# Optimization experiments

Hardware: AMD Instinct MI355X
Metric: run time of the kernel (lower is better)

The kernel has to match this reference:

```python
import jax, jax.numpy as jnp
import numpy as np

B, L, E, DK = 16, 2048, 1024, 128
MODE = "Decoder"


def setup_inputs() -> dict:
    key = jax.random.key(0)
    ks = jax.random.split(key, 6)
    x = jax.random.normal(ks[0], (B, L, E), dtype=jnp.float32)
    context = jax.random.normal(ks[1], (B, L, E), dtype=jnp.float32)
    batch_lengths = jax.random.randint(ks[2], (B,), 1, L + 1)  # valid lengths in [1, L]
    Wq = jax.random.normal(ks[3], (E, DK), dtype=jnp.float32) * 0.02
    Wk = jax.random.normal(ks[4], (E, DK), dtype=jnp.float32) * 0.02
    Wv = jax.random.normal(ks[5], (E, DK), dtype=jnp.float32) * 0.02
    return {"x": x, "context": context, "batch_lengths": batch_lengths,
            "Wq": Wq, "Wk": Wk, "Wv": Wv, "max_len": L}


def reference(x, context, batch_lengths, Wq, Wk, Wv, max_len):
    # x, context: [B, L, E]; batch_lengths: [B] ints; weights: [E, DK]
    Lq = x.shape[1]
    dk = Wq.shape[1]
    pos = jnp.arange(Lq)
    # outputMask: zero out padded time steps, broadcast over feature dim [B, L, 1]
    len_mask = (pos[None, :] < batch_lengths[:, None]).astype(x.dtype)[:, :, None]
    Q = (context @ Wq) * len_mask
    K = (context @ Wk) * len_mask
    V = (x @ Wv) * len_mask
    # energy: [B, Lq, Lk]
    energy = jnp.einsum("bqd,bkd->bqk", Q, K)
    # attnMask: -inf on padded key positions
    key_valid = pos[None, None, :] < batch_lengths[:, None, None]  # [B,1,Lk]
    if MODE == "Decoder":
        causal = pos[None, :, None] >= pos[None, None, :]  # j <= i
        key_valid = key_valid & causal
    energy = jnp.where(key_valid, energy, -jnp.inf)
    score = jax.nn.softmax(energy / jnp.sqrt(jnp.asarray(dk, x.dtype)), axis=-1)
    return jnp.einsum("bqk,bkd->bqd", score, V)
```

## Files before the change

kernel.cpp:

```cpp
#include <hip/hip_runtime.h>

#define DEV __device__ __forceinline__

typedef __attribute__((ext_vector_type(4))) float f32x4;
typedef __attribute__((ext_vector_type(4))) unsigned short u16x4;
typedef __attribute__((ext_vector_type(8))) __bf16 bf16x8;

constexpr int NB = 16, SL = 2048, EM = 1024, DKD = 128;

DEV unsigned short f2bf(float f) {
  unsigned int u = __float_as_uint(f);
  u += 0x7FFFu + ((u >> 16) & 1u);
  return (unsigned short)(u >> 16);
}

DEV f32x4 mfma16(bf16x8 a, bf16x8 b, f32x4 c) {
  return __builtin_amdgcn_mfma_f32_16x16x32_bf16(a, b, c, 0, 0, 0);
}

DEV void dma16(const void* g, void* l) {
  __builtin_amdgcn_global_load_lds(
      (const __attribute__((address_space(1))) unsigned int*)g,
      (__attribute__((address_space(3))) unsigned int*)l, 16, 0, 0);
}

DEV bf16x8 cvt8(f32x4 a, f32x4 b) {
  bf16x8 r;
  r[0] = (__bf16)a[0]; r[1] = (__bf16)a[1]; r[2] = (__bf16)a[2]; r[3] = (__bf16)a[3];
  r[4] = (__bf16)b[0]; r[5] = (__bf16)b[1]; r[6] = (__bf16)b[2]; r[7] = (__bf16)b[3];
  return r;
}

#define SBAR() __builtin_amdgcn_sched_barrier(0)

__global__ __launch_bounds__(256) void prep_w(
    const float* __restrict__ Wq, const float* __restrict__ Wk,
    const float* __restrict__ Wv, unsigned short* __restrict__ Wt,
    float* __restrict__ mvg)
{
  __shared__ unsigned short T[64 * 128];
  const int tid = threadIdx.x;
  if (blockIdx.x == 0) {
    #pragma unroll
    for (int i = 0; i < NB * DKD / 256; ++i) mvg[i * 256 + tid] = 0.f;
  }
  const int m = blockIdx.x >> 4, kc = blockIdx.x & 15;
  const float* W = (m == 0) ? Wq : ((m == 1) ? Wk : Wv);
  #pragma unroll
  for (int it = 0; it < 8; ++it) {
    int idx = it * 256 + tid;
    int kk = idx >> 5, n4 = (idx & 31) * 4;
    f32x4 w4 = *(const f32x4*)(W + (size_t)(kc * 64 + kk) * DKD + n4);
    *(u16x4*)&T[kk * 128 + n4] =
        u16x4{ f2bf(w4[0]), f2bf(w4[1]), f2bf(w4[2]), f2bf(w4[3]) };
  }
  __syncthreads();
  #pragma unroll
  for (int it = 0; it < 4; ++it) {
    int idx = it * 256 + tid;
    int p = idx & 7, n = idx >> 3;
    int c = p ^ (n & 7);
    unsigned short v[8];
    #pragma unroll
    for (int e = 0; e < 8; ++e) v[e] = T[(c * 8 + e) * 128 + n];
    size_t t = ((size_t)(m * 16 + kc) * 128 + n) * 8 + p;
    *(u16x4*)(Wt + t * 8)     = u16x4{v[0], v[1], v[2], v[3]};
    *(u16x4*)(Wt + t * 8 + 4) = u16x4{v[4], v[5], v[6], v[7]};
  }
}

__global__ __launch_bounds__(256, 2) void proj_qk(
    const float* __restrict__ ctx, const unsigned short* __restrict__ Wt,
    const int* __restrict__ lens, unsigned short* __restrict__ Qo,
    unsigned short* __restrict__ Kz)
{
  __shared__ float Als[2][64 * 64];
  const int tid = threadIdx.x;
  const int wave = tid >> 6, lane = tid & 63;
  const int quad = lane >> 4, mm = lane & 15;
  const int rb = blockIdx.x * 64;
  const int len = lens[blockIdx.x >> 5];
  if ((rb & (SL - 1)) >= len) return;

  f32x4 acc[4][4];
  #pragma unroll
  for (int i = 0; i < 4; ++i)
    #pragma unroll
    for (int j = 0; j < 4; ++j) acc[i][j] = f32x4{0.f, 0.f, 0.f, 0.f};

  const float* asrc[4];
  #pragma unroll
  for (int i = 0; i < 4; ++i) {
    const int rl_ = wave * 16 + i * 4 + (lane >> 4);
    const int cc  = (lane & 8) | ((lane & 7) ^ (rl_ & 7));
    asrc[i] = ctx + (size_t)(rb + rl_) * EM + cc * 4;
  }
  int soff[2][2];
  #pragma unroll
  for (int ks = 0; ks < 2; ++ks) {
    soff[ks][0] = (ks * 8 + ((quad * 2)     ^ (mm & 7))) * 4;
    soff[ks][1] = (ks * 8 + ((quad * 2 + 1) ^ (mm & 7))) * 4;
  }
  const unsigned short* bbase[4][2];
  #pragma unroll
  for (int lo = 0; lo < 4; ++lo)
    #pragma unroll
    for (int ks = 0; ks < 2; ++ks) {
      const int nrow = (wave * 4 + lo) * 16 + mm;
      const int pp = (ks * 4 + quad) ^ (mm & 7);
      const int cs = nrow * 8 + pp;
      bbase[lo][ks] = Wt + ((size_t)(cs >> 10) * 16384 + (cs & 1023)) * 8;
    }

  #pragma unroll
  for (int i = 0; i < 4; ++i)
    dma16(asrc[i],      (char*)Als[0] + wave * 4096 + i * 1024);
  #pragma unroll
  for (int i = 0; i < 4; ++i)
    dma16(asrc[i] + 64, (char*)Als[1] + wave * 4096 + i * 1024);
  __asm__ volatile("s_waitcnt vmcnt(4)" ::: "memory");
  __builtin_amdgcn_s_barrier();

  #pragma unroll 1
  for (int kc = 0; kc < 16; ++kc) {
    SBAR();
    bf16x8 bfr[4][2];
    #pragma unroll
    for (int lo = 0; lo < 4; ++lo)
      #pragma unroll
      for (int ks = 0; ks < 2; ++ks)
        bfr[lo][ks] = *(const bf16x8*)(bbase[lo][ks] + (size_t)kc * 8192);
    bf16x8 af[4][2];
    #pragma unroll
    for (int rt = 0; rt < 4; ++rt) {
      const float* rbase = Als[kc & 1] + (rt * 16 + mm) * 64;
      #pragma unroll
      for (int ks = 0; ks < 2; ++ks) {
        f32x4 a0 = *(const f32x4*)(rbase + soff[ks][0]);
        f32x4 a1 = *(const f32x4*)(rbase + soff[ks][1]);
        af[rt][ks] = cvt8(a0, a1);
      }
    }
    __asm__ volatile("s_waitcnt lgkmcnt(0)" ::: "memory");
    SBAR();
    __builtin_amdgcn_s_barrier();
    {
      const int kn = (kc + 2 < 16) ? (kc + 2) : 15;
      #pragma unroll
      for (int i = 0; i < 4; ++i)
        dma16(asrc[i] + kn * 64, (char*)Als[kc & 1] + wave * 4096 + i * 1024);
    }
    #pragma unroll
    for (int lo = 0; lo < 4; ++lo)
      #pragma unroll
      for (int ks = 0; ks < 2; ++ks)
        #pragma unroll
        for (int rt = 0; rt < 4; ++rt)
          acc[rt][lo] = mfma16(af[rt][ks], bfr[lo][ks], acc[rt][lo]);
    __builtin_amdgcn_s_barrier();
  }
  __asm__ volatile("s_waitcnt vmcnt(0)" ::: "memory");

  const float SCALE = 1.4426950408889634f * 0.08838834764831845f;
  #pragma unroll
  for (int rt = 0; rt < 4; ++rt)
    #pragma unroll
    for (int lo = 0; lo < 4; ++lo) {
      const int ctg = wave * 4 + lo;
      #pragma unroll
      for (int reg = 0; reg < 4; ++reg) {
        const int row = rb + rt * 16 + quad * 4 + reg;
        const int j = row & (SL - 1);
        const float val = acc[rt][lo][reg];
        if (ctg < 8) {
          const int d = ctg * 16 + mm;
          Qo[(size_t)row * DKD + d] = f2bf(val * ((j < len) ? SCALE : 0.f));
        } else {
          const int d = (ctg - 8) * 16 + mm;
          Kz[(size_t)row * DKD + (((d >> 3) ^ (j & 15)) * 8) + (d & 7)] = f2bf(val);
        }
      }
    }
}

__global__ __launch_bounds__(256, 2) void proj_v(
    const float* __restrict__ x, const unsigned short* __restrict__ Wt,
    const int* __restrict__ lens, unsigned short* __restrict__ Vz,
    float* __restrict__ mvg)
{
  __shared__ float Als[2][64 * 64];
  const int tid = threadIdx.x;
  const int wave = tid >> 6, lane = tid & 63;
  const int quad = lane >> 4, mm = lane & 15;
  const int rb = blockIdx.x * 64;
  const int bidx = blockIdx.x >> 5;
  const int len = lens[bidx];
  if ((rb & (SL - 1)) >= len) return;

  f32x4 acc[4][2];
  #pragma unroll
  for (int i = 0; i < 4; ++i) { acc[i][0] = f32x4{0.f,0.f,0.f,0.f}; acc[i][1] = f32x4{0.f,0.f,0.f,0.f}; }

  const float* asrc[4];
  #pragma unroll
  for (int i = 0; i < 4; ++i) {
    const int rl_ = wave * 16 + i * 4 + (lane >> 4);
    const int cc  = (lane & 8) | ((lane & 7) ^ (rl_ & 7));
    asrc[i] = x + (size_t)(rb + rl_) * EM + cc * 4;
  }
  int soff[2][2];
  #pragma unroll
  for (int ks = 0; ks < 2; ++ks) {
    soff[ks][0] = (ks * 8 + ((quad * 2)     ^ (mm & 7))) * 4;
    soff[ks][1] = (ks * 8 + ((quad * 2 + 1) ^ (mm & 7))) * 4;
  }
  const unsigned short* bbase[2][2];
  #pragma unroll
  for (int lo = 0; lo < 2; ++lo)
    #pragma unroll
    for (int ks = 0; ks < 2; ++ks) {
      const int nrow = (wave * 2 + lo) * 16 + mm;
      const int pp = (ks * 4 + quad) ^ (mm & 7);
      const int cs = nrow * 8 + pp;
      bbase[lo][ks] = Wt + ((size_t)2 * 16384 + cs) * 8;
    }

  #pragma unroll
  for (int i = 0; i < 4; ++i)
    dma16(asrc[i],      (char*)Als[0] + wave * 4096 + i * 1024);
  #pragma unroll
  for (int i = 0; i < 4; ++i)
    dma16(asrc[i] + 64, (char*)Als[1] + wave * 4096 + i * 1024);
  __asm__ volatile("s_waitcnt vmcnt(4)" ::: "memory");
  __builtin_amdgcn_s_barrier();

  #pragma unroll 1
  for (int kc = 0; kc < 16; ++kc) {
    SBAR();
    bf16x8 bfr[2][2];
    #pragma unroll
    for (int lo = 0; lo < 2; ++lo)
      #pragma unroll
      for (int ks = 0; ks < 2; ++ks)
        bfr[lo][ks] = *(const bf16x8*)(bbase[lo][ks] + (size_t)kc * 8192);
    bf16x8 af[4][2];
    #pragma unroll
    for (int rt = 0; rt < 4; ++rt) {
      const float* rbase = Als[kc & 1] + (rt * 16 + mm) * 64;
      #pragma unroll
      for (int ks = 0; ks < 2; ++ks) {
        f32x4 a0 = *(const f32x4*)(rbase + soff[ks][0]);
        f32x4 a1 = *(const f32x4*)(rbase + soff[ks][1]);
        af[rt][ks] = cvt8(a0, a1);
      }
    }
    __asm__ volatile("s_waitcnt lgkmcnt(0)" ::: "memory");
    SBAR();
    __builtin_amdgcn_s_barrier();
    {
      const int kn = (kc + 2 < 16) ? (kc + 2) : 15;
      #pragma unroll
      for (int i = 0; i < 4; ++i)
        dma16(asrc[i] + kn * 64, (char*)Als[kc & 1] + wave * 4096 + i * 1024);
    }
    #pragma unroll
    for (int lo = 0; lo < 2; ++lo)
      #pragma unroll
      for (int ks = 0; ks < 2; ++ks)
        #pragma unroll
        for (int rt = 0; rt < 4; ++rt)
          acc[rt][lo] = mfma16(af[rt][ks], bfr[lo][ks], acc[rt][lo]);
    __builtin_amdgcn_s_barrier();
  }
  __asm__ volatile("s_waitcnt vmcnt(0)" ::: "memory");

  #pragma unroll
  for (int rt = 0; rt < 4; ++rt)
    #pragma unroll
    for (int lo = 0; lo < 2; ++lo) {
      const int d = (wave * 2 + lo) * 16 + mm;
      const int row0 = rb + rt * 16 + quad * 4;
      const int b = row0 >> 11, j0 = row0 & (SL - 1);
      u16x4 pk = u16x4{ f2bf(acc[rt][lo][0]), f2bf(acc[rt][lo][1]),
                        f2bf(acc[rt][lo][2]), f2bf(acc[rt][lo][3]) };
      size_t off = (size_t)b * DKD * SL + (size_t)d * SL + (j0 & ~63)
                 + ((((j0 >> 3) & 7) ^ (d & 7)) * 8) + (j0 & 7);
      *(u16x4*)(Vz + off) = pk;
    }

  const int jb = rb & (SL - 1);
  #pragma unroll
  for (int lo = 0; lo < 2; ++lo) {
    const int d = (wave * 2 + lo) * 16 + mm;
    float part = 0.f;
    #pragma unroll
    for (int rt = 0; rt < 4; ++rt) {
      const int jr = jb + rt * 16 + quad * 4;
      #pragma unroll
      for (int reg = 0; reg < 4; ++reg)
        if (jr + reg < len) part += acc[rt][lo][reg];
    }
    part += __shfl_xor(part, 16);
    part += __shfl_xor(part, 32);
    if (quad == 0) atomicAdd(mvg + bidx * DKD + d, part);
  }
}

__global__ __launch_bounds__(256, 2) void attn(
    const unsigned short* __restrict__ Qw, const unsigned short* __restrict__ Kz,
    const unsigned short* __restrict__ Vz, const float* __restrict__ mvg,
    const int* __restrict__ lens, float* __restrict__ out)
{
  __shared__ unsigned short Ks[2][64 * 128];
  __shared__ unsigned short Vs[2][128 * 64];
  __shared__ unsigned short Ps[4][16 * 72];
  const int tid = threadIdx.x;
  const int wave = tid >> 6, lane = tid & 63;
  const int quad = lane >> 4, mm = lane & 15;
  const int b = blockIdx.y;
  const int qb = ((int)gridDim.x - 1 - (int)blockIdx.x) * 64;
  const int len = lens[b];

  if (qb >= len) {
    const int dd = (tid & 31) * 4;
    const int r0 = tid >> 5;
    const f32x4 m4 = *(const f32x4*)(mvg + b * DKD + dd);
    const float inv = 1.0f / (float)len;
    const f32x4 val = f32x4{ m4[0]*inv, m4[1]*inv, m4[2]*inv, m4[3]*inv };
    #pragma unroll
    for (int it = 0; it < 8; ++it) {
      const int row = qb + it * 8 + r0;
      *(f32x4*)(out + ((size_t)b * SL + row) * DKD + dd) = val;
    }
    return;
  }

  const int kend = min(qb + 64, len);
  const int nblk = (kend + 63) >> 6;
  const int irow0 = qb + wave * 16 + quad * 4;

  bf16x8 aQ[4];
  {
    const unsigned short* qbase =
        Qw + (size_t)(b * SL + qb + wave * 16 + mm) * DKD + quad * 8;
    #pragma unroll
    for (int cc = 0; cc < 4; ++cc) aQ[cc] = *(const bf16x8*)(qbase + cc * 32);
  }
  bf16x8 onesb;
  #pragma unroll
  for (int i = 0; i < 8; ++i) onesb[i] = (__bf16)1.0f;

  float mr[4];
  #pragma unroll
  for (int r = 0; r < 4; ++r) mr[r] = -__builtin_inff();
  f32x4 acc[8];
  #pragma unroll
  for (int i = 0; i < 8; ++i) acc[i] = f32x4{0.f,0.f,0.f,0.f};
  f32x4 accl = f32x4{0.f,0.f,0.f,0.f};

  #pragma unroll
  for (int it = 0; it < 4; ++it) {
    int s = it * 256 + tid;
    dma16(Kz + (size_t)(b * SL) * DKD + (size_t)s * 8,
          (char*)Ks[0] + (it * 256 + wave * 64) * 16);
  }
  #pragma unroll
  for (int it = 0; it < 4; ++it) {
    int s = it * 256 + tid;
    int d = s >> 3, p = s & 7;
    dma16(Vz + (size_t)b * DKD * SL + (size_t)d * SL + p * 8,
          (char*)Vs[0] + (it * 256 + wave * 64) * 16);
  }

  #pragma unroll 1
  for (int blk = 0; blk < nblk; ++blk) {
    const int kb = blk * 64;
    __syncthreads();
    if (blk + 1 < nblk) {
      const int kb1 = kb + 64;
      const int nb = (blk + 1) & 1;
      #pragma unroll
      for (int it = 0; it < 4; ++it) {
        int s = it * 256 + tid;
        dma16(Kz + (size_t)(b * SL + kb1) * DKD + (size_t)s * 8,
              (char*)Ks[nb] + (it * 256 + wave * 64) * 16);
      }
      #pragma unroll
      for (int it = 0; it < 4; ++it) {
        int s = it * 256 + tid;
        int d = s >> 3, p = s & 7;
        dma16(Vz + (size_t)b * DKD * SL + (size_t)d * SL + kb1 + p * 8,
              (char*)Vs[nb] + (it * 256 + wave * 64) * 16);
      }
    }
    const unsigned short* kbuf = Ks[blk & 1];
    const unsigned short* vbuf = Vs[blk & 1];

    f32x4 s4[4];
    #pragma unroll
    for (int nt = 0; nt < 4; ++nt) {
      f32x4 c = f32x4{0.f,0.f,0.f,0.f};
      const int j = nt * 16 + mm;
      #pragma unroll
      for (int cc = 0; cc < 4; ++cc) {
        const int pp = (cc * 4 + quad) ^ mm;
        bf16x8 kf = *(const bf16x8*)(kbuf + j * 128 + pp * 8);
        c = mfma16(aQ[cc], kf, c);
      }
      s4[nt] = c;
    }

    float alpha[4];
    #pragma unroll
    for (int reg = 0; reg < 4; ++reg) {
      const int jl = min(irow0 + reg + 1, len);
      float v0 = (kb + mm      < jl) ? s4[0][reg] : -__builtin_inff();
      float v1 = (kb + 16 + mm < jl) ? s4[1][reg] : -__builtin_inff();
      float v2 = (kb + 32 + mm < jl) ? s4[2][reg] : -__builtin_inff();
      float v3 = (kb + 48 + mm < jl) ? s4[3][reg] : -__builtin_inff();
      float mx = fmaxf(fmaxf(v0, v1), fmaxf(v2, v3));
      #pragma unroll
      for (int xm = 1; xm < 16; xm <<= 1) mx = fmaxf(mx, __shfl_xor(mx, xm));
      const float mn = fmaxf(mr[reg], mx);
      alpha[reg] = __builtin_amdgcn_exp2f(mr[reg] - mn);
      const float p0 = __builtin_amdgcn_exp2f(v0 - mn);
      const float p1 = __builtin_amdgcn_exp2f(v1 - mn);
      const float p2 = __builtin_amdgcn_exp2f(v2 - mn);
      const float p3 = __builtin_amdgcn_exp2f(v3 - mn);
      mr[reg] = mn;
      const int prow = quad * 4 + reg;
      Ps[wave][prow * 72 + mm]      = f2bf(p0);
      Ps[wave][prow * 72 + 16 + mm] = f2bf(p1);
      Ps[wave][prow * 72 + 32 + mm] = f2bf(p2);
      Ps[wave][prow * 72 + 48 + mm] = f2bf(p3);
    }
    #pragma unroll
    for (int nt = 0; nt < 8; ++nt) {
      f32x4 a = acc[nt];
      a[0] *= alpha[0]; a[1] *= alpha[1]; a[2] *= alpha[2]; a[3] *= alpha[3];
      acc[nt] = a;
    }
    accl[0] *= alpha[0]; accl[1] *= alpha[1];
    accl[2] *= alpha[2]; accl[3] *= alpha[3];
    __asm__ volatile("s_waitcnt lgkmcnt(0)" ::: "memory");
    bf16x8 aP[2];
    #pragma unroll
    for (int ks = 0; ks < 2; ++ks)
      aP[ks] = *(const bf16x8*)(&Ps[wave][mm * 72 + ks * 32 + quad * 8]);
    #pragma unroll
    for (int ks = 0; ks < 2; ++ks) {
      #pragma unroll
      for (int nt = 0; nt < 8; ++nt) {
        const int pp = (ks * 4 + quad) ^ (mm & 7);
        bf16x8 vf = *(const bf16x8*)(vbuf + (nt * 16 + mm) * 64 + pp * 8);
        acc[nt] = mfma16(aP[ks], vf, acc[nt]);
      }
      accl = mfma16(aP[ks], onesb, accl);
    }
  }

  #pragma unroll
  for (int reg = 0; reg < 4; ++reg) {
    const float rl = 1.0f / accl[reg];
    const size_t base = ((size_t)b * SL + irow0 + reg) * DKD + mm;
    #pragma unroll
    for (int nt = 0; nt < 8; ++nt)
      out[base + nt * 16] = acc[nt][reg] * rl;
  }
}

extern "C" void kernel_launch(void* const* d_in, const int* in_sizes, int n_in,
                              void* d_out, int out_size, void* d_ws, size_t ws_size,
                              hipStream_t stream) {
  const float* x    = (const float*)d_in[0];
  const float* ctx  = (const float*)d_in[1];
  const int*   lens = (const int*)d_in[2];
  const float* Wq   = (const float*)d_in[3];
  const float* Wk   = (const float*)d_in[4];
  const float* Wv   = (const float*)d_in[5];
  float* out = (float*)d_out;

  const size_t QKV = (size_t)NB * SL * DKD * sizeof(unsigned short);
  const size_t WTSZ = (size_t)3 * 16 * 128 * 8 * 8 * sizeof(unsigned short);
  const size_t MVSZ = (size_t)NB * DKD * sizeof(float);
  if (ws_size < 3 * QKV + WTSZ + MVSZ) return;
  unsigned short* Qws = (unsigned short*)d_ws;
  unsigned short* Kzs = (unsigned short*)((char*)d_ws + QKV);
  unsigned short* Vzs = (unsigned short*)((char*)d_ws + 2 * QKV);
  unsigned short* Wt  = (unsigned short*)((char*)d_ws + 3 * QKV);
  float*          mvg = (float*)((char*)d_ws + 3 * QKV + WTSZ);

  prep_w <<<dim3(48), 256, 0, stream>>>(Wq, Wk, Wv, Wt, mvg);
  proj_qk<<<dim3(NB * SL / 64), 256, 0, stream>>>(ctx, Wt, lens, Qws, Kzs);
  proj_v <<<dim3(NB * SL / 64), 256, 0, stream>>>(x, Wt, lens, Vzs, mvg);
  attn   <<<dim3(SL / 64, NB), 256, 0, stream>>>(Qws, Kzs, Vzs, mvg, lens, out);
}
```

Measured before the change: 346.8 us.

## Split attention keys across two wave groups and drop LDS staging in projections

The projection kernels stop staging activations in LDS through DMA and barriers. Each wave now loads fp32 rows from global memory into registers with one-step prefetch and uses a 2x2 wave tiling over rows and columns. The attention kernel goes to 512 threads: two wave groups each handle half of a 128-key block, and their partial softmax states are merged through LDS at the end. It also adds s_setprio around the MFMA sections and clamps the running max so fully masked halves do not produce NaN. The cost is more LDS for K/V and more register pressure, and projection reads lose LDS reuse and may be less coalesced.

```diff
diff --git a/kernel.cpp b/kernel.cpp
--- a/kernel.cpp
+++ b/kernel.cpp
@@ -30,8 +30,6 @@
   r[4] = (__bf16)b[0]; r[5] = (__bf16)b[1]; r[6] = (__bf16)b[2]; r[7] = (__bf16)b[3];
   return r;
 }
-
-#define SBAR() __builtin_amdgcn_sched_barrier(0)
 
 __global__ __launch_bounds__(256) void prep_w(
     const float* __restrict__ Wq, const float* __restrict__ Wk,
@@ -74,109 +72,83 @@
     const int* __restrict__ lens, unsigned short* __restrict__ Qo,
     unsigned short* __restrict__ Kz)
 {
-  __shared__ float Als[2][64 * 64];
   const int tid = threadIdx.x;
   const int wave = tid >> 6, lane = tid & 63;
   const int quad = lane >> 4, mm = lane & 15;
+  const int mh = wave >> 1, nh = wave & 1;
   const int rb = blockIdx.x * 64;
   const int len = lens[blockIdx.x >> 5];
   if ((rb & (SL - 1)) >= len) return;
 
-  f32x4 acc[4][4];
-  #pragma unroll
-  for (int i = 0; i < 4; ++i)
-    #pragma unroll
-    for (int j = 0; j < 4; ++j) acc[i][j] = f32x4{0.f, 0.f, 0.f, 0.f};
-
-  const float* asrc[4];
-  #pragma unroll
-  for (int i = 0; i < 4; ++i) {
-    const int rl_ = wave * 16 + i * 4 + (lane >> 4);
-    const int cc  = (lane & 8) | ((lane & 7) ^ (rl_ & 7));
-    asrc[i] = ctx + (size_t)(rb + rl_) * EM + cc * 4;
-  }
-  int soff[2][2];
-  #pragma unroll
-  for (int ks = 0; ks < 2; ++ks) {
-    soff[ks][0] = (ks * 8 + ((quad * 2)     ^ (mm & 7))) * 4;
-    soff[ks][1] = (ks * 8 + ((quad * 2 + 1) ^ (mm & 7))) * 4;
-  }
-  const unsigned short* bbase[4][2];
-  #pragma unroll
-  for (int lo = 0; lo < 4; ++lo)
+  f32x4 acc[2][8];
+  #pragma unroll
+  for (int rt = 0; rt < 2; ++rt)
+    #pragma unroll
+    for (int nt = 0; nt < 8; ++nt) acc[rt][nt] = f32x4{0.f, 0.f, 0.f, 0.f};
+
+  const float* arow[2];
+  #pragma unroll
+  for (int rt = 0; rt < 2; ++rt)
+    arow[rt] = ctx + (size_t)(rb + mh * 32 + rt * 16 + mm) * EM + quad * 8;
+
+  const int pl0 = (quad)     ^ (mm & 7);
+  const int pl1 = (4 + quad) ^ (mm & 7);
+  const unsigned short* bb = Wt + (size_t)nh * 131072 + mm * 64;
+
+  f32x4 An[2][2][2];
+  #pragma unroll
+  for (int rt = 0; rt < 2; ++rt)
     #pragma unroll
     for (int ks = 0; ks < 2; ++ks) {
-      const int nrow = (wave * 4 + lo) * 16 + mm;
-      const int pp = (ks * 4 + quad) ^ (mm & 7);
-      const int cs = nrow * 8 + pp;
-      bbase[lo][ks] = Wt + ((size_t)(cs >> 10) * 16384 + (cs & 1023)) * 8;
-    }
-
-  #pragma unroll
-  for (int i = 0; i < 4; ++i)
-    dma16(asrc[i],      (char*)Als[0] + wave * 4096 + i * 1024);
-  #pragma unroll
-  for (int i = 0; i < 4; ++i)
-    dma16(asrc[i] + 64, (char*)Als[1] + wave * 4096 + i * 1024);
-  __asm__ volatile("s_waitcnt vmcnt(4)" ::: "memory");
-  __builtin_amdgcn_s_barrier();
+      An[rt][ks][0] = *(const f32x4*)(arow[rt] + ks * 32);
+      An[rt][ks][1] = *(const f32x4*)(arow[rt] + ks * 32 + 4);
+    }
 
   #pragma unroll 1
   for (int kc = 0; kc < 16; ++kc) {
-    SBAR();
-    bf16x8 bfr[4][2];
-    #pragma unroll
-    for (int lo = 0; lo < 4; ++lo)
+    bf16x8 af[2][2];
+    #pragma unroll
+    for (int rt = 0; rt < 2; ++rt)
       #pragma unroll
       for (int ks = 0; ks < 2; ++ks)
-        bfr[lo][ks] = *(const bf16x8*)(bbase[lo][ks] + (size_t)kc * 8192);
-    bf16x8 af[4][2];
-    #pragma unroll
-    for (int rt = 0; rt < 4; ++rt) {
-      const float* rbase = Als[kc & 1] + (rt * 16 + mm) * 64;
-      #pragma unroll
-      for (int ks = 0; ks < 2; ++ks) {
-        f32x4 a0 = *(const f32x4*)(rbase + soff[ks][0]);
-        f32x4 a1 = *(const f32x4*)(rbase + soff[ks][1]);
-        af[rt][ks] = cvt8(a0, a1);
-      }
-    }
-    __asm__ volatile("s_waitcnt lgkmcnt(0)" ::: "memory");
-    SBAR();
-    __builtin_amdgcn_s_barrier();
-    {
-      const int kn = (kc + 2 < 16) ? (kc + 2) : 15;
-      #pragma unroll
-      for (int i = 0; i < 4; ++i)
-        dma16(asrc[i] + kn * 64, (char*)Als[kc & 1] + wave * 4096 + i * 1024);
-    }
-    #pragma unroll
-    for (int lo = 0; lo < 4; ++lo)
-      #pragma unroll
-      for (int ks = 0; ks < 2; ++ks)
+        af[rt][ks] = cvt8(An[rt][ks][0], An[rt][ks][1]);
+    if (kc < 15) {
+      #pragma unroll
+      for (int rt = 0; rt < 2; ++rt)
         #pragma unroll
-        for (int rt = 0; rt < 4; ++rt)
-          acc[rt][lo] = mfma16(af[rt][ks], bfr[lo][ks], acc[rt][lo]);
-    __builtin_amdgcn_s_barrier();
-  }
-  __asm__ volatile("s_waitcnt vmcnt(0)" ::: "memory");
+        for (int ks = 0; ks < 2; ++ks) {
+          An[rt][ks][0] = *(const f32x4*)(arow[rt] + (kc + 1) * 64 + ks * 32);
+          An[rt][ks][1] = *(const f32x4*)(arow[rt] + (kc + 1) * 64 + ks * 32 + 4);
+        }
+    }
+    const unsigned short* bk = bb + (size_t)kc * 8192;
+    #pragma unroll
+    for (int nt = 0; nt < 8; ++nt) {
+      bf16x8 b0 = *(const bf16x8*)(bk + nt * 1024 + pl0 * 8);
+      bf16x8 b1 = *(const bf16x8*)(bk + nt * 1024 + pl1 * 8);
+      #pragma unroll
+      for (int rt = 0; rt < 2; ++rt)
+        acc[rt][nt] = mfma16(af[rt][0], b0, acc[rt][nt]);
+      #pragma unroll
+      for (int rt = 0; rt < 2; ++rt)
+        acc[rt][nt] = mfma16(af[rt][1], b1, acc[rt][nt]);
+    }
+  }
 
   const float SCALE = 1.4426950408889634f * 0.08838834764831845f;
   #pragma unroll
-  for (int rt = 0; rt < 4; ++rt)
-    #pragma unroll
-    for (int lo = 0; lo < 4; ++lo) {
-      const int ctg = wave * 4 + lo;
+  for (int rt = 0; rt < 2; ++rt)
+    #pragma unroll
+    for (int nt = 0; nt < 8; ++nt) {
       #pragma unroll
       for (int reg = 0; reg < 4; ++reg) {
-        const int row = rb + rt * 16 + quad * 4 + reg;
+        const int row = rb + mh * 32 + rt * 16 + quad * 4 + reg;
         const int j = row & (SL - 1);
-        const float val = acc[rt][lo][reg];
-        if (ctg < 8) {
-          const int d = ctg * 16 + mm;
+        const float val = acc[rt][nt][reg];
+        const int d = nt * 16 + mm;
+        if (nh == 0) {
           Qo[(size_t)row * DKD + d] = f2bf(val * ((j < len) ? SCALE : 0.f));
         } else {
-          const int d = (ctg - 8) * 16 + mm;
           Kz[(size_t)row * DKD + (((d >> 3) ^ (j & 15)) * 8) + (d & 7)] = f2bf(val);
         }
       }
@@ -188,101 +160,79 @@
     const int* __restrict__ lens, unsigned short* __restrict__ Vz,
     float* __restrict__ mvg)
 {
-  __shared__ float Als[2][64 * 64];
   const int tid = threadIdx.x;
   const int wave = tid >> 6, lane = tid & 63;
   const int quad = lane >> 4, mm = lane & 15;
+  const int mh = wave >> 1, nh = wave & 1;
   const int rb = blockIdx.x * 64;
   const int bidx = blockIdx.x >> 5;
   const int len = lens[bidx];
   if ((rb & (SL - 1)) >= len) return;
 
-  f32x4 acc[4][2];
-  #pragma unroll
-  for (int i = 0; i < 4; ++i) { acc[i][0] = f32x4{0.f,0.f,0.f,0.f}; acc[i][1] = f32x4{0.f,0.f,0.f,0.f}; }
-
-  const float* asrc[4];
-  #pragma unroll
-  for (int i = 0; i < 4; ++i) {
-    const int rl_ = wave * 16 + i * 4 + (lane >> 4);
-    const int cc  = (lane & 8) | ((lane & 7) ^ (rl_ & 7));
-    asrc[i] = x + (size_t)(rb + rl_) * EM + cc * 4;
-  }
-  int soff[2][2];
-  #pragma unroll
-  for (int ks = 0; ks < 2; ++ks) {
-    soff[ks][0] = (ks * 8 + ((quad * 2)     ^ (mm & 7))) * 4;
-    soff[ks][1] = (ks * 8 + ((quad * 2 + 1) ^ (mm & 7))) * 4;
-  }
-  const unsigned short* bbase[2][2];
-  #pragma unroll
-  for (int lo = 0; lo < 2; ++lo)
+  f32x4 acc[2][4];
+  #pragma unroll
+  for (int rt = 0; rt < 2; ++rt)
+    #pragma unroll
+    for (int nt = 0; nt < 4; ++nt) acc[rt][nt] = f32x4{0.f, 0.f, 0.f, 0.f};
+
+  const float* arow[2];
+  #pragma unroll
+  for (int rt = 0; rt < 2; ++rt)
+    arow[rt] = x + (size_t)(rb + mh * 32 + rt * 16 + mm) * EM + quad * 8;
+
+  const int pl0 = (quad)     ^ (mm & 7);
+  const int pl1 = (4 + quad) ^ (mm & 7);
+  const unsigned short* bb = Wt + (size_t)2 * 131072 + (size_t)nh * 4096 + mm * 64;
+
+  f32x4 An[2][2][2];
+  #pragma unroll
+  for (int rt = 0; rt < 2; ++rt)
     #pragma unroll
     for (int ks = 0; ks < 2; ++ks) {
-      const int nrow = (wave * 2 + lo) * 16 + mm;
-      const int pp = (ks * 4 + quad) ^ (mm & 7);
-      const int cs = nrow * 8 + pp;
-      bbase[lo][ks] = Wt + ((size_t)2 * 16384 + cs) * 8;
-    }
-
-  #pragma unroll
-  for (int i = 0; i < 4; ++i)
-    dma16(asrc[i],      (char*)Als[0] + wave * 4096 + i * 1024);
-  #pragma unroll
-  for (int i = 0; i < 4; ++i)
-    dma16(asrc[i] + 64, (char*)Als[1] + wave * 4096 + i * 1024);
-  __asm__ volatile("s_waitcnt vmcnt(4)" ::: "memory");
-  __builtin_amdgcn_s_barrier();
+      An[rt][ks][0] = *(const f32x4*)(arow[rt] + ks * 32);
+      An[rt][ks][1] = *(const f32x4*)(arow[rt] + ks * 32 + 4);
+    }
 
   #pragma unroll 1
   for (int kc = 0; kc < 16; ++kc) {
-    SBAR();
-    bf16x8 bfr[2][2];
-    #pragma unroll
-    for (int lo = 0; lo < 2; ++lo)
+    bf16x8 af[2][2];
+    #pragma unroll
+    for (int rt = 0; rt < 2; ++rt)
       #pragma unroll
       for (int ks = 0; ks < 2; ++ks)
-        bfr[lo][ks] = *(const bf16x8*)(bbase[lo][ks] + (size_t)kc * 8192);
-    bf16x8 af[4][2];
-    #pragma unroll
-    for (int rt = 0; rt < 4; ++rt) {
-      const float* rbase = Als[kc & 1] + (rt * 16 + mm) * 64;
-      #pragma unroll
-      for (int ks = 0; ks < 2; ++ks) {
-        f32x4 a0 = *(const f32x4*)(rbase + soff[ks][0]);
-        f32x4 a1 = *(const f32x4*)(rbase + soff[ks][1]);
-        af[rt][ks] = cvt8(a0, a1);
-      }
-    }
-    __asm__ volatile("s_waitcnt lgkmcnt(0)" ::: "memory");
-    SBAR();
-    __builtin_amdgcn_s_barrier();
-    {
-      const int kn = (kc + 2 < 16) ? (kc + 2) : 15;
-      #pragma unroll
-      for (int i = 0; i < 4; ++i)
-        dma16(asrc[i] + kn * 64, (char*)Als[kc & 1] + wave * 4096 + i * 1024);
-    }
-    #pragma unroll
-    for (int lo = 0; lo < 2; ++lo)
-      #pragma unroll
-      for (int ks = 0; ks < 2; ++ks)
+        af[rt][ks] = cvt8(An[rt][ks][0], An[rt][ks][1]);
+    if (kc < 15) {
+      #pragma unroll
+      for (int rt = 0; rt < 2; ++rt)
         #pragma unroll
-        for (int rt = 0; rt < 4; ++rt)
-          acc[rt][lo] = mfma16(af[rt][ks], bfr[lo][ks], acc[rt][lo]);
-    __builtin_amdgcn_s_barrier();
-  }
-  __asm__ volatile("s_waitcnt vmcnt(0)" ::: "memory");
-
-  #pragma unroll
-  for (int rt = 0; rt < 4; ++rt)
-    #pragma unroll
-    for (int lo = 0; lo < 2; ++lo) {
-      const int d = (wave * 2 + lo) * 16 + mm;
-      const int row0 = rb + rt * 16 + quad * 4;
+        for (int ks = 0; ks < 2; ++ks) {
+          An[rt][ks][0] = *(const f32x4*)(arow[rt] + (kc + 1) * 64 + ks * 32);
+          An[rt][ks][1] = *(const f32x4*)(arow[rt] + (kc + 1) * 64 + ks * 32 + 4);
+        }
+    }
+    const unsigned short* bk = bb + (size_t)kc * 8192;
+    #pragma unroll
+    for (int nt = 0; nt < 4; ++nt) {
+      bf16x8 b0 = *(const bf16x8*)(bk + nt * 1024 + pl0 * 8);
+      bf16x8 b1 = *(const bf16x8*)(bk + nt * 1024 + pl1 * 8);
+      #pragma unroll
+      for (int rt = 0; rt < 2; ++rt)
+        acc[rt][nt] = mfma16(af[rt][0], b0, acc[rt][nt]);
+      #pragma unroll
+      for (int rt = 0; rt < 2; ++rt)
+        acc[rt][nt] = mfma16(af[rt][1], b1, acc[rt][nt]);
+    }
+  }
+
+  #pragma unroll
+  for (int rt = 0; rt < 2; ++rt)
+    #pragma unroll
+    for (int nt = 0; nt < 4; ++nt) {
+      const int d = nh * 64 + nt * 16 + mm;
+      const int row0 = rb + mh * 32 + rt * 16 + quad * 4;
       const int b = row0 >> 11, j0 = row0 & (SL - 1);
-      u16x4 pk = u16x4{ f2bf(acc[rt][lo][0]), f2bf(acc[rt][lo][1]),
-                        f2bf(acc[rt][lo][2]), f2bf(acc[rt][lo][3]) };
+      u16x4 pk = u16x4{ f2bf(acc[rt][nt][0]), f2bf(acc[rt][nt][1]),
+                        f2bf(acc[rt][nt][2]), f2bf(acc[rt][nt][3]) };
       size_t off = (size_t)b * DKD * SL + (size_t)d * SL + (j0 & ~63)
                  + ((((j0 >> 3) & 7) ^ (d & 7)) * 8) + (j0 & 7);
       *(u16x4*)(Vz + off) = pk;
@@ -290,15 +240,15 @@
 
   const int jb = rb & (SL - 1);
   #pragma unroll
-  for (int lo = 0; lo < 2; ++lo) {
-    const int d = (wave * 2 + lo) * 16 + mm;
+  for (int nt = 0; nt < 4; ++nt) {
+    const int d = nh * 64 + nt * 16 + mm;
     float part = 0.f;
     #pragma unroll
-    for (int rt = 0; rt < 4; ++rt) {
-      const int jr = jb + rt * 16 + quad * 4;
+    for (int rt = 0; rt < 2; ++rt) {
+      const int jr = jb + mh * 32 + rt * 16 + quad * 4;
       #pragma unroll
       for (int reg = 0; reg < 4; ++reg)
-        if (jr + reg < len) part += acc[rt][lo][reg];
+        if (jr + reg < len) part += acc[rt][nt][reg];
     }
     part += __shfl_xor(part, 16);
     part += __shfl_xor(part, 32);
@@ -306,17 +256,19 @@
   }
 }
 
-__global__ __launch_bounds__(256, 2) void attn(
+__global__ __launch_bounds__(512, 2) void attn(
     const unsigned short* __restrict__ Qw, const unsigned short* __restrict__ Kz,
     const unsigned short* __restrict__ Vz, const float* __restrict__ mvg,
     const int* __restrict__ lens, float* __restrict__ out)
 {
-  __shared__ unsigned short Ks[2][64 * 128];
-  __shared__ unsigned short Vs[2][128 * 64];
-  __shared__ unsigned short Ps[4][16 * 72];
+  __shared__ unsigned short Ks[2][128 * 128];
+  __shared__ unsigned short Vs[2][2][128 * 64];
+  __shared__ unsigned short Ps[8][16 * 72];
   const int tid = threadIdx.x;
   const int wave = tid >> 6, lane = tid & 63;
   const int quad = lane >> 4, mm = lane & 15;
+  const int wg = wave & 3;
+  const int wh = wave >> 2;
   const int b = blockIdx.y;
   const int qb = ((int)gridDim.x - 1 - (int)blockIdx.x) * 64;
   const int len = lens[b];
@@ -328,21 +280,21 @@
     const float inv = 1.0f / (float)len;
     const f32x4 val = f32x4{ m4[0]*inv, m4[1]*inv, m4[2]*inv, m4[3]*inv };
     #pragma unroll
-    for (int it = 0; it < 8; ++it) {
-      const int row = qb + it * 8 + r0;
+    for (int it = 0; it < 4; ++it) {
+      const int row = qb + it * 16 + r0;
       *(f32x4*)(out + ((size_t)b * SL + row) * DKD + dd) = val;
     }
     return;
   }
 
   const int kend = min(qb + 64, len);
-  const int nblk = (kend + 63) >> 6;
-  const int irow0 = qb + wave * 16 + quad * 4;
+  const int nblk = (kend + 127) >> 7;
+  const int irow0 = qb + wg * 16 + quad * 4;
 
   bf16x8 aQ[4];
   {
     const unsigned short* qbase =
-        Qw + (size_t)(b * SL + qb + wave * 16 + mm) * DKD + quad * 8;
+        Qw + (size_t)(b * SL + qb + wg * 16 + mm) * DKD + quad * 8;
     #pragma unroll
     for (int cc = 0; cc < 4; ++cc) aQ[cc] = *(const bf16x8*)(qbase + cc * 32);
   }
@@ -360,47 +312,53 @@
 
   #pragma unroll
   for (int it = 0; it < 4; ++it) {
-    int s = it * 256 + tid;
+    int s = it * 512 + tid;
     dma16(Kz + (size_t)(b * SL) * DKD + (size_t)s * 8,
-          (char*)Ks[0] + (it * 256 + wave * 64) * 16);
-  }
-  #pragma unroll
-  for (int it = 0; it < 4; ++it) {
-    int s = it * 256 + tid;
-    int d = s >> 3, p = s & 7;
-    dma16(Vz + (size_t)b * DKD * SL + (size_t)d * SL + p * 8,
-          (char*)Vs[0] + (it * 256 + wave * 64) * 16);
-  }
+          (char*)Ks[0] + (it * 512 + wave * 64) * 16);
+  }
+  #pragma unroll
+  for (int h = 0; h < 2; ++h)
+    #pragma unroll
+    for (int it = 0; it < 2; ++it) {
+      int s = it * 512 + tid;
+      int d = s >> 3, p = s & 7;
+      dma16(Vz + (size_t)b * DKD * SL + (size_t)d * SL + h * 64 + p * 8,
+            (char*)Vs[0][h] + (it * 512 + wave * 64) * 16);
+    }
 
   #pragma unroll 1
   for (int blk = 0; blk < nblk; ++blk) {
-    const int kb = blk * 64;
+    const int kb = blk * 128;
     __syncthreads();
     if (blk + 1 < nblk) {
-      const int kb1 = kb + 64;
+      const int kb1 = kb + 128;
       const int nb = (blk + 1) & 1;
       #pragma unroll
       for (int it = 0; it < 4; ++it) {
-        int s = it * 256 + tid;
+        int s = it * 512 + tid;
         dma16(Kz + (size_t)(b * SL + kb1) * DKD + (size_t)s * 8,
-              (char*)Ks[nb] + (it * 256 + wave * 64) * 16);
+              (char*)Ks[nb] + (it * 512 + wave * 64) * 16);
       }
       #pragma unroll
-      for (int it = 0; it < 4; ++it) {
-        int s = it * 256 + tid;
-        int d = s >> 3, p = s & 7;
-        dma16(Vz + (size_t)b * DKD * SL + (size_t)d * SL + kb1 + p * 8,
-              (char*)Vs[nb] + (it * 256 + wave * 64) * 16);
-      }
+      for (int h = 0; h < 2; ++h)
+        #pragma unroll
+        for (int it = 0; it < 2; ++it) {
+          int s = it * 512 + tid;
+          int d = s >> 3, p = s & 7;
+          dma16(Vz + (size_t)b * DKD * SL + (size_t)d * SL + (kb1 + h * 64) + p * 8,
+                (char*)Vs[nb][h] + (it * 512 + wave * 64) * 16);
+        }
     }
     const unsigned short* kbuf = Ks[blk & 1];
-    const unsigned short* vbuf = Vs[blk & 1];
+    const unsigned short* vbuf = Vs[blk & 1][wh];
+    const int kbh = kb + wh * 64;
 
     f32x4 s4[4];
+    __builtin_amdgcn_s_setprio(1);
     #pragma unroll
     for (int nt = 0; nt < 4; ++nt) {
       f32x4 c = f32x4{0.f,0.f,0.f,0.f};
-      const int j = nt * 16 + mm;
+      const int j = wh * 64 + nt * 16 + mm;
       #pragma unroll
       for (int cc = 0; cc < 4; ++cc) {
         const int pp = (cc * 4 + quad) ^ mm;
@@ -409,19 +367,20 @@
       }
       s4[nt] = c;
     }
+    __builtin_amdgcn_s_setprio(0);
 
     float alpha[4];
     #pragma unroll
     for (int reg = 0; reg < 4; ++reg) {
       const int jl = min(irow0 + reg + 1, len);
-      float v0 = (kb + mm      < jl) ? s4[0][reg] : -__builtin_inff();
-      float v1 = (kb + 16 + mm < jl) ? s4[1][reg] : -__builtin_inff();
-      float v2 = (kb + 32 + mm < jl) ? s4[2][reg] : -__builtin_inff();
-      float v3 = (kb + 48 + mm < jl) ? s4[3][reg] : -__builtin_inff();
+      float v0 = (kbh + mm      < jl) ? s4[0][reg] : -__builtin_inff();
+      float v1 = (kbh + 16 + mm < jl) ? s4[1][reg] : -__builtin_inff();
+      float v2 = (kbh + 32 + mm < jl) ? s4[2][reg] : -__builtin_inff();
+      float v3 = (kbh + 48 + mm < jl) ? s4[3][reg] : -__builtin_inff();
       float mx = fmaxf(fmaxf(v0, v1), fmaxf(v2, v3));
       #pragma unroll
       for (int xm = 1; xm < 16; xm <<= 1) mx = fmaxf(mx, __shfl_xor(mx, xm));
-      const float mn = fmaxf(mr[reg], mx);
+      const float mn = fmaxf(fmaxf(mr[reg], mx), -1e30f);
       alpha[reg] = __builtin_amdgcn_exp2f(mr[reg] - mn);
       const float p0 = __builtin_amdgcn_exp2f(v0 - mn);
       const float p1 = __builtin_amdgcn_exp2f(v1 - mn);
@@ -447,6 +406,7 @@
     #pragma unroll
     for (int ks = 0; ks < 2; ++ks)
       aP[ks] = *(const bf16x8*)(&Ps[wave][mm * 72 + ks * 32 + quad * 8]);
+    __builtin_amdgcn_s_setprio(1);
     #pragma unroll
     for (int ks = 0; ks < 2; ++ks) {
       #pragma unroll
@@ -457,15 +417,37 @@
       }
       accl = mfma16(aP[ks], onesb, accl);
     }
-  }
-
-  #pragma unroll
-  for (int reg = 0; reg < 4; ++reg) {
-    const float rl = 1.0f / accl[reg];
-    const size_t base = ((size_t)b * SL + irow0 + reg) * DKD + mm;
+    __builtin_amdgcn_s_setprio(0);
+  }
+
+  __syncthreads();
+  float* mrg = (float*)&Ks[0][0];
+  if (wh == 1) {
+    float* p = mrg + (wg * 64 + lane) * 41;
+    #pragma unroll
+    for (int r = 0; r < 4; ++r) p[r] = mr[r];
+    #pragma unroll
+    for (int r = 0; r < 4; ++r) p[4 + r] = accl[r];
     #pragma unroll
     for (int nt = 0; nt < 8; ++nt)
-      out[base + nt * 16] = acc[nt][reg] * rl;
+      #pragma unroll
+      for (int r = 0; r < 4; ++r) p[8 + nt * 4 + r] = acc[nt][r];
+  }
+  __syncthreads();
+  if (wh == 0) {
+    const float* p = mrg + (wg * 64 + lane) * 41;
+    #pragma unroll
+    for (int reg = 0; reg < 4; ++reg) {
+      const float m1 = p[reg], l1 = p[4 + reg];
+      const float m = fmaxf(mr[reg], m1);
+      const float f0 = __builtin_amdgcn_exp2f(mr[reg] - m);
+      const float f1 = __builtin_amdgcn_exp2f(m1 - m);
+      const float rl = 1.0f / (accl[reg] * f0 + l1 * f1);
+      const size_t base = ((size_t)b * SL + irow0 + reg) * DKD + mm;
+      #pragma unroll
+      for (int nt = 0; nt < 8; ++nt)
+        out[base + nt * 16] = (acc[nt][reg] * f0 + p[8 + nt * 4 + reg] * f1) * rl;
+    }
   }
 }
 
@@ -493,5 +475,5 @@
   prep_w <<<dim3(48), 256, 0, stream>>>(Wq, Wk, Wv, Wt, mvg);
   proj_qk<<<dim3(NB * SL / 64), 256, 0, stream>>>(ctx, Wt, lens, Qws, Kzs);
   proj_v <<<dim3(NB * SL / 64), 256, 0, stream>>>(x, Wt, lens, Vzs, mvg);
-  attn   <<<dim3(SL / 64, NB), 256, 0, stream>>>(Qws, Kzs, Vzs, mvg, lens, out);
-}
+  attn   <<<dim3(SL / 64, NB), 512, 0, stream>>>(Qws, Kzs, Vzs, mvg, lens, out);
+}
```

Result: slower. 388.4 us (+12.0%).
